# Optimization experiments

Hardware: AMD Instinct MI355X
Metric: run time of the kernel (lower is better)

Reference implementation:

```python
import jax, jax.numpy as jnp
import numpy as np

N_NODES = 100000


def _gcn_layer(x, src, dst, ew, norm_s, norm_d, W, b):
    # DGL GraphConv with edge weights, norm='both':
    # h_v = D_in(v)^-1/2 * sum_{(u,v) in E} w_uv * D_out(u)^-1/2 * x_u; then Linear.
    m = (x * norm_s[:, None])[src] * ew[:, None]        # [E, d] gather + weight
    agg = jax.ops.segment_sum(m, dst, num_segments=N_NODES)  # [N, d] scatter-add
    return (agg * norm_d[:, None]) @ W + b


def setup_inputs() -> dict:
    key = jax.random.key(0)
    ks = jax.random.split(key, 12)
    N, E, D, C = N_NODES, 1600000, 64, 32
    inp = {
        "x": jax.random.normal(ks[0], (N, D), jnp.float32),
        "src": jax.random.randint(ks[1], (E,), 0, N, jnp.int64),
        "dst": jax.random.randint(ks[2], (E,), 0, N, jnp.int64),
        "ew": jax.random.uniform(ks[3], (E,), jnp.float32),
    }
    s = 1.0 / np.sqrt(D)
    for i, k in zip(range(1, 5), ks[4:8]):
        inp[f"W{i}"] = jax.random.normal(k, (D, D), jnp.float32) * s
        inp[f"b{i}"] = jnp.zeros((D,), jnp.float32)
    inp["Wr"] = jax.random.normal(ks[8], (D, D), jnp.float32) * s
    inp["br"] = jnp.zeros((D,), jnp.float32)
    inp["Wo"] = jax.random.normal(ks[9], (D, C), jnp.float32) * s
    inp["bo"] = jnp.zeros((C,), jnp.float32)
    return inp


def reference(x, src, dst, ew, W1, b1, W2, b2, W3, b3, W4, b4, Wr, br, Wo, bo):
    ones = jnp.ones(src.shape, x.dtype)
    deg_out = jnp.clip(jax.ops.segment_sum(ones, src, num_segments=N_NODES), 1.0)
    deg_in = jnp.clip(jax.ops.segment_sum(ones, dst, num_segments=N_NODES), 1.0)
    norm_s = deg_out ** -0.5
    norm_d = deg_in ** -0.5

    res = x @ Wr + br
    h = jax.nn.relu(_gcn_layer(x, src, dst, ew, norm_s, norm_d, W1, b1))
    h = jax.nn.relu(_gcn_layer(h, src, dst, ew, norm_s, norm_d, W2, b2))
    h = jax.nn.relu(_gcn_layer(h, src, dst, ew, norm_s, norm_d, W3, b3))
    h = _gcn_layer(h, src, dst, ew, norm_s, norm_d, W4, b4)
    h = jax.nn.relu(h + res)
    return h @ Wo + bo
```

## Files before the change

### kernel.cpp

```cpp
#include <hip/hip_runtime.h>

#define NN 100000
#define D 64
#define G 3
#define RS 33334
#define NC 85
#define NB (G*NC)

typedef short bf16x8 __attribute__((ext_vector_type(8)));
typedef float f32x4 __attribute__((ext_vector_type(4)));
typedef float f32x2 __attribute__((ext_vector_type(2)));

__device__ __forceinline__ float bf2f_lo(unsigned w) { return __uint_as_float(w << 16); }
__device__ __forceinline__ float bf2f_hi(unsigned w) { return __uint_as_float(w & 0xffff0000u); }
__device__ __forceinline__ unsigned short f2bf(float f) {
    unsigned u = __float_as_uint(f);
    return (unsigned short)((u + 0x7fffu + ((u >> 16) & 1u)) >> 16);
}
__device__ __forceinline__ unsigned pack2(float a, float b) {
    return (unsigned)f2bf(a) | ((unsigned)f2bf(b) << 16);
}
__device__ __forceinline__ unsigned char f2fp8(float v) {
    return (unsigned char)(__builtin_amdgcn_cvt_pk_fp8_f32(v, v, 0, false) & 0xff);
}
__device__ __forceinline__ unsigned pack_cw(int s, float w) {
    return ((unsigned)f2bf(w) << 17) | (unsigned)s;
}
#define PKFMA(acc, w2, p) \
    asm("v_pk_fma_f32 %0, %1, %2, %0" : "+v"(acc) : "v"(w2), "v"(p))

__global__ __launch_bounds__(1024) void k_hist(const int* __restrict__ src,
                                               const int* __restrict__ dst,
                                               unsigned short* __restrict__ psd, int E) {
    __shared__ unsigned h[RS / 2];
    int b = blockIdx.x, t = threadIdx.x;
    int g = b / NC, c = b - g * NC;
    int lo = g * RS;
    for (int i = t; i < RS / 2; i += 1024) h[i] = 0;
    __syncthreads();
    int e0 = (int)((((long long)c * E / NC)) & ~3LL);
    int e1 = (c == NC - 1) ? E : (int)((((long long)(c + 1) * E / NC)) & ~3LL);
    int m = (e1 - e0) & ~4095;
    for (int e = e0 + t * 4; e < e0 + m; e += 4096) {
        int4 s4 = *(const int4*)(src + e);
        int4 d4 = *(const int4*)(dst + e);
        int v;
        v = s4.x - lo; if ((unsigned)v < RS) atomicAdd(&h[v >> 1], 1u << ((v & 1) * 16));
        v = s4.y - lo; if ((unsigned)v < RS) atomicAdd(&h[v >> 1], 1u << ((v & 1) * 16));
        v = s4.z - lo; if ((unsigned)v < RS) atomicAdd(&h[v >> 1], 1u << ((v & 1) * 16));
        v = s4.w - lo; if ((unsigned)v < RS) atomicAdd(&h[v >> 1], 1u << ((v & 1) * 16));
        v = d4.x - lo; if ((unsigned)v < RS) atomicAdd(&h[v >> 1], 1u << ((v & 1) * 16 + 8));
        v = d4.y - lo; if ((unsigned)v < RS) atomicAdd(&h[v >> 1], 1u << ((v & 1) * 16 + 8));
        v = d4.z - lo; if ((unsigned)v < RS) atomicAdd(&h[v >> 1], 1u << ((v & 1) * 16 + 8));
        v = d4.w - lo; if ((unsigned)v < RS) atomicAdd(&h[v >> 1], 1u << ((v & 1) * 16 + 8));
    }
    for (int e = e0 + m + t; e < e1; e += 1024) {
        int v = src[e] - lo; if ((unsigned)v < RS) atomicAdd(&h[v >> 1], 1u << ((v & 1) * 16));
        v = dst[e] - lo;     if ((unsigned)v < RS) atomicAdd(&h[v >> 1], 1u << ((v & 1) * 16 + 8));
    }
    __syncthreads();
    unsigned* pb = (unsigned*)(psd + (size_t)b * RS);
    for (int i = t; i < RS / 2; i += 1024) pb[i] = h[i];
}

__global__ __launch_bounds__(1024) void k_scan1m(const unsigned short* __restrict__ psd,
                                                 float* __restrict__ ns, float* __restrict__ nd,
                                                 int* __restrict__ rowptr,
                                                 int* __restrict__ bsum, int n) {
    __shared__ int lds[1024];
    int t = threadIdx.x;
    int i = blockIdx.x * 1024 + t;
    int sv = 0, dv = 0;
    if (i < n) {
        int g = i / RS, off = i - g * RS;
        const unsigned short* p = psd + (size_t)(g * NC) * RS + off;
        #pragma unroll 5
        for (int c = 0; c < NC; ++c) {
            unsigned v = p[(size_t)c * RS];
            sv += (int)(v & 0xffu);
            dv += (int)(v >> 8);
        }
        ns[i] = rsqrtf(fmaxf((float)sv, 1.0f));
        nd[i] = rsqrtf(fmaxf((float)dv, 1.0f));
    }
    lds[t] = dv;
    __syncthreads();
    for (int off = 1; off < 1024; off <<= 1) {
        int v = lds[t];
        int a = (t >= off) ? lds[t - off] : 0;
        __syncthreads();
        lds[t] = v + a;
        __syncthreads();
    }
    if (t == 1023) bsum[blockIdx.x] = lds[1023];
    if (i < n) rowptr[i] = lds[t] - dv;
}

__global__ void k_scan3c(int* __restrict__ rowptr, const int* __restrict__ bsum,
                         const unsigned short* __restrict__ psd,
                         unsigned short* __restrict__ cur16,
                         int n, int E, int nb) {
    __shared__ int sbs[128];
    int t = threadIdx.x;
    if (t < 128) sbs[t] = (t < nb) ? bsum[t] : 0;
    __syncthreads();
    for (int off = 1; off < 128; off <<= 1) {
        int v = 0, a = 0;
        if (t < 128) { v = sbs[t]; if (t >= off) a = sbs[t - off]; }
        __syncthreads();
        if (t < 128) sbs[t] = v + a;
        __syncthreads();
    }
    int i = blockIdx.x * blockDim.x + t;
    if (i == 0) rowptr[n] = E;
    if (i >= n) return;
    int blk = i >> 10;
    int base = (blk > 0) ? sbs[blk - 1] : 0;
    int r = rowptr[i] + base;
    rowptr[i] = r;
    int g = i / RS, off = i - g * RS;
    const unsigned short* p = psd + (size_t)(g * NC) * RS + off;
    unsigned short* cp = cur16 + (size_t)(g * NC) * RS + off;
    int run = 0;
    #pragma unroll 5
    for (int c = 0; c < NC; ++c) {
        cp[(size_t)c * RS] = (unsigned short)run;
        run += (int)(p[(size_t)c * RS] >> 8);
    }
}

__global__ __launch_bounds__(1024) void k_fillsort(const int* __restrict__ src,
                                                   const int* __restrict__ dst,
                                                   const float* __restrict__ ew,
                                                   const int* __restrict__ rowptr,
                                                   const unsigned short* __restrict__ cur16,
                                                   unsigned* __restrict__ cw, int E) {
    __shared__ int cur[RS];
    int b = blockIdx.x, t = threadIdx.x;
    int g = b / NC, c = b - g * NC;
    int lo = g * RS;
    const unsigned short* c16 = cur16 + (size_t)b * RS;
    for (int i = t; i < RS; i += 1024) cur[i] = rowptr[lo + i] + (int)c16[i];
    __syncthreads();
    int e0 = (int)((((long long)c * E / NC)) & ~3LL);
    int e1 = (c == NC - 1) ? E : (int)((((long long)(c + 1) * E / NC)) & ~3LL);
    int m = (e1 - e0) & ~4095;
    for (int e = e0 + t * 4; e < e0 + m; e += 4096) {
        int4 s4 = *(const int4*)(src + e);
        int4 d4 = *(const int4*)(dst + e);
        float4 w4 = *(const float4*)(ew + e);
        int d;
        d = d4.x - lo; if ((unsigned)d < RS) { int p = atomicAdd(&cur[d], 1); cw[p] = pack_cw(s4.x, w4.x); }
        d = d4.y - lo; if ((unsigned)d < RS) { int p = atomicAdd(&cur[d], 1); cw[p] = pack_cw(s4.y, w4.y); }
        d = d4.z - lo; if ((unsigned)d < RS) { int p = atomicAdd(&cur[d], 1); cw[p] = pack_cw(s4.z, w4.z); }
        d = d4.w - lo; if ((unsigned)d < RS) { int p = atomicAdd(&cur[d], 1); cw[p] = pack_cw(s4.w, w4.w); }
    }
    for (int e = e0 + m + t; e < e1; e += 1024) {
        int d = dst[e] - lo;
        if ((unsigned)d < RS) {
            int p = atomicAdd(&cur[d], 1);
            cw[p] = pack_cw(src[e], ew[e]);
        }
    }
}

__global__ __launch_bounds__(256) void k_gemm2(const float* __restrict__ x,
                                               const float* __restrict__ Wr,
                                               const float* __restrict__ brs,
                                               const float* __restrict__ W1,
                                               const float* __restrict__ ns,
                                               unsigned short* __restrict__ resb,
                                               unsigned char* __restrict__ tmat, int n) {
    __shared__ unsigned short WTr[64][72];
    __shared__ unsigned short WT1[64][72];
    int t = threadIdx.x;
    for (int i = t; i < 64 * 64; i += 256) {
        int k = i >> 6, nn = i & 63;
        WTr[nn][k] = f2bf(Wr[i]);
        WT1[nn][k] = f2bf(W1[i]);
    }
    __syncthreads();
    int w = t >> 6, lane = t & 63;
    int m = lane & 15, q = lane >> 4;
    int node0 = blockIdx.x * 64 + w * 16;
    int nodeA = min(node0 + m, n - 1);
    const float* inf = x + (size_t)nodeA * D;
    float sc = ns[nodeA];
    bf16x8 afr[2], afs[2];
    #pragma unroll
    for (int kc = 0; kc < 2; ++kc) {
        float4 f0 = *(const float4*)(inf + kc * 32 + q * 8);
        float4 f1 = *(const float4*)(inf + kc * 32 + q * 8 + 4);
        union { bf16x8 v; unsigned short u[8]; } ta, ts;
        ta.u[0] = f2bf(f0.x); ta.u[1] = f2bf(f0.y);
        ta.u[2] = f2bf(f0.z); ta.u[3] = f2bf(f0.w);
        ta.u[4] = f2bf(f1.x); ta.u[5] = f2bf(f1.y);
        ta.u[6] = f2bf(f1.z); ta.u[7] = f2bf(f1.w);
        ts.u[0] = f2bf(f0.x * sc); ts.u[1] = f2bf(f0.y * sc);
        ts.u[2] = f2bf(f0.z * sc); ts.u[3] = f2bf(f0.w * sc);
        ts.u[4] = f2bf(f1.x * sc); ts.u[5] = f2bf(f1.y * sc);
        ts.u[6] = f2bf(f1.z * sc); ts.u[7] = f2bf(f1.w * sc);
        afr[kc] = ta.v;
        afs[kc] = ts.v;
    }
    #pragma unroll
    for (int nt = 0; nt < 4; ++nt) {
        f32x4 ar = {0.f, 0.f, 0.f, 0.f};
        f32x4 at = {0.f, 0.f, 0.f, 0.f};
        #pragma unroll
        for (int kc = 0; kc < 2; ++kc) {
            union { bf16x8 v; uint4 u; } bfr, bf1;
            bfr.u = *(const uint4*)&WTr[nt * 16 + m][kc * 32 + q * 8];
            bf1.u = *(const uint4*)&WT1[nt * 16 + m][kc * 32 + q * 8];
            ar = __builtin_amdgcn_mfma_f32_16x16x32_bf16(afr[kc], bfr.v, ar, 0, 0, 0);
            at = __builtin_amdgcn_mfma_f32_16x16x32_bf16(afs[kc], bf1.v, at, 0, 0, 0);
        }
        int col = nt * 16 + m;
        float bb = brs[col];
        #pragma unroll
        for (int r = 0; r < 4; ++r) {
            int node = node0 + q * 4 + r;
            if (node < n) {
                resb[(size_t)node * D + col] = f2bf(ar[r] + bb);
                tmat[(size_t)node * D + col] = f2fp8(at[r]);
            }
        }
    }
}

template<bool LAST>
__global__ void k_gather(const int* __restrict__ rowptr, const unsigned* __restrict__ cw,
                         const unsigned char* __restrict__ tmat,
                         const float* __restrict__ nd, const float* __restrict__ ns,
                         const float* __restrict__ bias,
                         const unsigned short* __restrict__ resb,
                         unsigned short* __restrict__ outb, int n, int E) {
    int grp = threadIdx.x >> 3;
    int h   = threadIdx.x & 7;
    int node = blockIdx.x * 32 + grp;
    bool valid = node < n;
    int nc = valid ? node : 0;
    int beg = rowptr[nc];
    int end = valid ? rowptr[nc + 1] : beg;
    unsigned h8 = (unsigned)(h * 8);
    f32x2 A0={0.f,0.f},A1={0.f,0.f},A2={0.f,0.f},A3={0.f,0.f};
    f32x2 C0={0.f,0.f},C1={0.f,0.f},C2={0.f,0.f},C3={0.f,0.f};
    unsigned cv0 = (beg     < end) ? cw[beg]     : 0u;
    unsigned cv1 = (beg + 1 < end) ? cw[beg + 1] : 0u;
    unsigned cv2 = (beg + 2 < end) ? cw[beg + 2] : 0u;
    unsigned cv3 = (beg + 3 < end) ? cw[beg + 3] : 0u;
    unsigned cv4 = (beg + 4 < end) ? cw[beg + 4] : 0u;
    unsigned cv5 = (beg + 5 < end) ? cw[beg + 5] : 0u;
    unsigned cv6 = (beg + 6 < end) ? cw[beg + 6] : 0u;
    unsigned cv7 = (beg + 7 < end) ? cw[beg + 7] : 0u;
    for (int e = beg; e < end; e += 8) {
        uint2 r0 = *(const uint2*)(tmat + (((cv0 & 0x1FFFFu) << 6) + h8));
        uint2 r1 = *(const uint2*)(tmat + (((cv1 & 0x1FFFFu) << 6) + h8));
        uint2 r2 = *(const uint2*)(tmat + (((cv2 & 0x1FFFFu) << 6) + h8));
        uint2 r3 = *(const uint2*)(tmat + (((cv3 & 0x1FFFFu) << 6) + h8));
        uint2 r4 = *(const uint2*)(tmat + (((cv4 & 0x1FFFFu) << 6) + h8));
        uint2 r5 = *(const uint2*)(tmat + (((cv5 & 0x1FFFFu) << 6) + h8));
        uint2 r6 = *(const uint2*)(tmat + (((cv6 & 0x1FFFFu) << 6) + h8));
        uint2 r7 = *(const uint2*)(tmat + (((cv7 & 0x1FFFFu) << 6) + h8));
        float w0 = __uint_as_float((cv0 >> 17) << 16);
        float w1 = __uint_as_float((cv1 >> 17) << 16);
        float w2 = __uint_as_float((cv2 >> 17) << 16);
        float w3 = __uint_as_float((cv3 >> 17) << 16);
        float w4 = __uint_as_float((cv4 >> 17) << 16);
        float w5 = __uint_as_float((cv5 >> 17) << 16);
        float w6 = __uint_as_float((cv6 >> 17) << 16);
        float w7 = __uint_as_float((cv7 >> 17) << 16);
        int f = e + 8;
        cv0 = (f     < end) ? cw[f]     : 0u;
        cv1 = (f + 1 < end) ? cw[f + 1] : 0u;
        cv2 = (f + 2 < end) ? cw[f + 2] : 0u;
        cv3 = (f + 3 < end) ? cw[f + 3] : 0u;
        cv4 = (f + 4 < end) ? cw[f + 4] : 0u;
        cv5 = (f + 5 < end) ? cw[f + 5] : 0u;
        cv6 = (f + 6 < end) ? cw[f + 6] : 0u;
        cv7 = (f + 7 < end) ? cw[f + 7] : 0u;
        f32x2 p, wv;
        wv.x = w0; wv.y = w0;
        p = __builtin_amdgcn_cvt_pk_f32_fp8(r0.x, false); PKFMA(A0, wv, p);
        p = __builtin_amdgcn_cvt_pk_f32_fp8(r0.x, true);  PKFMA(A1, wv, p);
        p = __builtin_amdgcn_cvt_pk_f32_fp8(r0.y, false); PKFMA(A2, wv, p);
        p = __builtin_amdgcn_cvt_pk_f32_fp8(r0.y, true);  PKFMA(A3, wv, p);
        wv.x = w1; wv.y = w1;
        p = __builtin_amdgcn_cvt_pk_f32_fp8(r1.x, false); PKFMA(C0, wv, p);
        p = __builtin_amdgcn_cvt_pk_f32_fp8(r1.x, true);  PKFMA(C1, wv, p);
        p = __builtin_amdgcn_cvt_pk_f32_fp8(r1.y, false); PKFMA(C2, wv, p);
        p = __builtin_amdgcn_cvt_pk_f32_fp8(r1.y, true);  PKFMA(C3, wv, p);
        wv.x = w2; wv.y = w2;
        p = __builtin_amdgcn_cvt_pk_f32_fp8(r2.x, false); PKFMA(A0, wv, p);
        p = __builtin_amdgcn_cvt_pk_f32_fp8(r2.x, true);  PKFMA(A1, wv, p);
        p = __builtin_amdgcn_cvt_pk_f32_fp8(r2.y, false); PKFMA(A2, wv, p);
        p = __builtin_amdgcn_cvt_pk_f32_fp8(r2.y, true);  PKFMA(A3, wv, p);
        wv.x = w3; wv.y = w3;
        p = __builtin_amdgcn_cvt_pk_f32_fp8(r3.x, false); PKFMA(C0, wv, p);
        p = __builtin_amdgcn_cvt_pk_f32_fp8(r3.x, true);  PKFMA(C1, wv, p);
        p = __builtin_amdgcn_cvt_pk_f32_fp8(r3.y, false); PKFMA(C2, wv, p);
        p = __builtin_amdgcn_cvt_pk_f32_fp8(r3.y, true);  PKFMA(C3, wv, p);
        wv.x = w4; wv.y = w4;
        p = __builtin_amdgcn_cvt_pk_f32_fp8(r4.x, false); PKFMA(A0, wv, p);
        p = __builtin_amdgcn_cvt_pk_f32_fp8(r4.x, true);  PKFMA(A1, wv, p);
        p = __builtin_amdgcn_cvt_pk_f32_fp8(r4.y, false); PKFMA(A2, wv, p);
        p = __builtin_amdgcn_cvt_pk_f32_fp8(r4.y, true);  PKFMA(A3, wv, p);
        wv.x = w5; wv.y = w5;
        p = __builtin_amdgcn_cvt_pk_f32_fp8(r5.x, false); PKFMA(C0, wv, p);
        p = __builtin_amdgcn_cvt_pk_f32_fp8(r5.x, true);  PKFMA(C1, wv, p);
        p = __builtin_amdgcn_cvt_pk_f32_fp8(r5.y, false); PKFMA(C2, wv, p);
        p = __builtin_amdgcn_cvt_pk_f32_fp8(r5.y, true);  PKFMA(C3, wv, p);
        wv.x = w6; wv.y = w6;
        p = __builtin_amdgcn_cvt_pk_f32_fp8(r6.x, false); PKFMA(A0, wv, p);
        p = __builtin_amdgcn_cvt_pk_f32_fp8(r6.x, true);  PKFMA(A1, wv, p);
        p = __builtin_amdgcn_cvt_pk_f32_fp8(r6.y, false); PKFMA(A2, wv, p);
        p = __builtin_amdgcn_cvt_pk_f32_fp8(r6.y, true);  PKFMA(A3, wv, p);
        wv.x = w7; wv.y = w7;
        p = __builtin_amdgcn_cvt_pk_f32_fp8(r7.x, false); PKFMA(C0, wv, p);
        p = __builtin_amdgcn_cvt_pk_f32_fp8(r7.x, true);  PKFMA(C1, wv, p);
        p = __builtin_amdgcn_cvt_pk_f32_fp8(r7.y, false); PKFMA(C2, wv, p);
        p = __builtin_amdgcn_cvt_pk_f32_fp8(r7.y, true);  PKFMA(C3, wv, p);
    }
    if (!valid) return;
    float a0 = A0.x + C0.x, a1 = A0.y + C0.y;
    float a2 = A1.x + C1.x, a3 = A1.y + C1.y;
    float a4 = A2.x + C2.x, a5 = A2.y + C2.y;
    float a6 = A3.x + C3.x, a7 = A3.y + C3.y;
    float ndv = nd[node];
    float4 b0 = *(const float4*)(bias + 8 * h);
    float4 b1 = *(const float4*)(bias + 8 * h + 4);
    float v0 = ndv * a0 + b0.x, v1 = ndv * a1 + b0.y;
    float v2 = ndv * a2 + b0.z, v3 = ndv * a3 + b0.w;
    float v4 = ndv * a4 + b1.x, v5 = ndv * a5 + b1.y;
    float v6 = ndv * a6 + b1.z, v7 = ndv * a7 + b1.w;
    if (LAST) {
        uint4 r = *((const uint4*)(resb + (size_t)node * D) + h);
        v0 += bf2f_lo(r.x); v1 += bf2f_hi(r.x);
        v2 += bf2f_lo(r.y); v3 += bf2f_hi(r.y);
        v4 += bf2f_lo(r.z); v5 += bf2f_hi(r.z);
        v6 += bf2f_lo(r.w); v7 += bf2f_hi(r.w);
    }
    v0 = fmaxf(v0, 0.f); v1 = fmaxf(v1, 0.f); v2 = fmaxf(v2, 0.f); v3 = fmaxf(v3, 0.f);
    v4 = fmaxf(v4, 0.f); v5 = fmaxf(v5, 0.f); v6 = fmaxf(v6, 0.f); v7 = fmaxf(v7, 0.f);
    if (!LAST) {
        float s = ns[node];
        v0 *= s; v1 *= s; v2 *= s; v3 *= s; v4 *= s; v5 *= s; v6 *= s; v7 *= s;
    }
    uint4 o = make_uint4(pack2(v0, v1), pack2(v2, v3), pack2(v4, v5), pack2(v6, v7));
    *((uint4*)(outb + (size_t)node * D) + h) = o;
}

template<int OUTD, bool BIAS, int OUTMODE>
__global__ __launch_bounds__(256) void k_gemm(const unsigned short* __restrict__ inb,
                                              const float* __restrict__ W,
                                              const float* __restrict__ bias,
                                              void* __restrict__ out_, int n) {
    constexpr int NT = OUTD / 16;
    __shared__ unsigned short WT[OUTD][72];
    int t = threadIdx.x;
    for (int i = t; i < 64 * OUTD; i += 256) {
        int k = i / OUTD, nn = i % OUTD;
        WT[nn][k] = f2bf(W[i]);
    }
    __syncthreads();
    int w = t >> 6, lane = t & 63;
    int m = lane & 15, q = lane >> 4;
    int node0 = blockIdx.x * 64 + w * 16;
    int nodeA = min(node0 + m, n - 1);
    const unsigned short* ip = inb + (size_t)nodeA * D;
    bf16x8 afr[2];
    #pragma unroll
    for (int kc = 0; kc < 2; ++kc) {
        union { bf16x8 v; uint4 u; } tmp;
        tmp.u = *(const uint4*)(ip + kc * 32 + q * 8);
        afr[kc] = tmp.v;
    }
    #pragma unroll
    for (int nt = 0; nt < NT; ++nt) {
        f32x4 acc = {0.f, 0.f, 0.f, 0.f};
        #pragma unroll
        for (int kc = 0; kc < 2; ++kc) {
            union { bf16x8 v; uint4 u; } bfr;
            bfr.u = *(const uint4*)&WT[nt * 16 + m][kc * 32 + q * 8];
            acc = __builtin_amdgcn_mfma_f32_16x16x32_bf16(afr[kc], bfr.v, acc, 0, 0, 0);
        }
        int col = nt * 16 + m;
        float bb = BIAS ? bias[col] : 0.f;
        #pragma unroll
        for (int r = 0; r < 4; ++r) {
            int node = node0 + q * 4 + r;
            if (node < n) {
                float v = acc[r] + bb;
                if (OUTMODE == 2)
                    ((unsigned char*)out_)[(size_t)node * OUTD + col] = f2fp8(v);
                else
                    ((float*)out_)[(size_t)node * OUTD + col] = v;
            }
        }
    }
}

static inline char* align_up(char* p, size_t a) {
    return (char*)(((uintptr_t)p + a - 1) & ~(uintptr_t)(a - 1));
}

extern "C" void kernel_launch(void* const* d_in, const int* in_sizes, int n_in,
                              void* d_out, int out_size, void* d_ws, size_t ws_size,
                              hipStream_t stream) {
    const float* x   = (const float*)d_in[0];
    const int*   src = (const int*)d_in[1];
    const int*   dst = (const int*)d_in[2];
    const float* ew  = (const float*)d_in[3];
    const float* Wl[4] = {(const float*)d_in[4], (const float*)d_in[6],
                          (const float*)d_in[8], (const float*)d_in[10]};
    const float* bl[4] = {(const float*)d_in[5], (const float*)d_in[7],
                          (const float*)d_in[9], (const float*)d_in[11]};
    const float* Wr = (const float*)d_in[12];
    const float* br = (const float*)d_in[13];
    const float* Wo = (const float*)d_in[14];
    const float* bo = (const float*)d_in[15];
    float* out = (float*)d_out;

    const int N = NN;
    const int E = in_sizes[1];

    char* p = (char*)d_ws;
    float* norm_s = (float*)p;            p = align_up(p + N * 4, 256);
    float* norm_d = (float*)p;            p = align_up(p + N * 4, 256);
    int*   rowptr = (int*)p;              p = align_up(p + (size_t)(G * RS + 80) * 4, 256);
    int*   bsum   = (int*)p;              p = align_up(p + 128 * 4, 256);
    unsigned* cw  = (unsigned*)p;         p = align_up(p + (size_t)E * 4, 256);
    unsigned short* psd   = (unsigned short*)p; p = align_up(p + (size_t)NB * RS * 2, 256);
    unsigned short* cur16 = (unsigned short*)p; p = align_up(p + (size_t)NB * RS * 2, 256);
    unsigned short* resb  = (unsigned short*)p; p = align_up(p + (size_t)N * D * 2, 256);
    unsigned short* xs   = psd;
    unsigned char*  tmat = (unsigned char*)(xs + (size_t)N * D);

    k_hist<<<NB, 1024, 0, stream>>>(src, dst, psd, E);
    int nb = (N + 1023) / 1024;
    k_scan1m<<<nb, 1024, 0, stream>>>(psd, norm_s, norm_d, rowptr, bsum, N);
    k_scan3c<<<(N + 255) / 256, 256, 0, stream>>>(rowptr, bsum, psd, cur16, N, E, nb);
    k_fillsort<<<NB, 1024, 0, stream>>>(src, dst, ew, rowptr, cur16, cw, E);

    k_gemm2<<<(N + 63) / 64, 256, 0, stream>>>(x, Wr, br, Wl[0], norm_s, resb, tmat, N);

    k_gather<false><<<(N + 31) / 32, 256, 0, stream>>>(
        rowptr, cw, tmat, norm_d, norm_s, bl[0], nullptr, xs, N, E);
    k_gemm<64, false, 2><<<(N + 63) / 64, 256, 0, stream>>>(xs, Wl[1], nullptr, tmat, N);
    k_gather<false><<<(N + 31) / 32, 256, 0, stream>>>(
        rowptr, cw, tmat, norm_d, norm_s, bl[1], nullptr, xs, N, E);
    k_gemm<64, false, 2><<<(N + 63) / 64, 256, 0, stream>>>(xs, Wl[2], nullptr, tmat, N);
    k_gather<false><<<(N + 31) / 32, 256, 0, stream>>>(
        rowptr, cw, tmat, norm_d, norm_s, bl[2], nullptr, xs, N, E);
    k_gemm<64, false, 2><<<(N + 63) / 64, 256, 0, stream>>>(xs, Wl[3], nullptr, tmat, N);
    k_gather<true><<<(N + 31) / 32, 256, 0, stream>>>(
        rowptr, cw, tmat, norm_d, nullptr, bl[3], resb, xs, N, E);
    k_gemm<32, true, 0><<<(N + 63) / 64, 256, 0, stream>>>(xs, Wo, bo, out, N);
}
```

Before: 307.7 us.

## Pad CSR rows to multiples of eight to drop bounds checks in gather

```diff
diff --git a/kernel.cpp b/kernel.cpp
--- a/kernel.cpp
+++ b/kernel.cpp
@@ -83,7 +83,8 @@
         ns[i] = rsqrtf(fmaxf((float)sv, 1.0f));
         nd[i] = rsqrtf(fmaxf((float)dv, 1.0f));
     }
-    lds[t] = dv;
+    int dvp = (dv + 7) & ~7;
+    lds[t] = dvp;
     __syncthreads();
     for (int off = 1; off < 1024; off <<= 1) {
         int v = lds[t];
@@ -93,13 +94,14 @@
         __syncthreads();
     }
     if (t == 1023) bsum[blockIdx.x] = lds[1023];
-    if (i < n) rowptr[i] = lds[t] - dv;
+    if (i < n) rowptr[i] = lds[t] - dvp;
 }
 
 __global__ void k_scan3c(int* __restrict__ rowptr, const int* __restrict__ bsum,
                          const unsigned short* __restrict__ psd,
                          unsigned short* __restrict__ cur16,
-                         int n, int E, int nb) {
+                         unsigned* __restrict__ cw,
+                         int n, int nb) {
     __shared__ int sbs[128];
     int t = threadIdx.x;
     if (t < 128) sbs[t] = (t < nb) ? bsum[t] : 0;
@@ -112,7 +114,7 @@
         __syncthreads();
     }
     int i = blockIdx.x * blockDim.x + t;
-    if (i == 0) rowptr[n] = E;
+    if (i == 0) rowptr[n] = sbs[127];
     if (i >= n) return;
     int blk = i >> 10;
     int base = (blk > 0) ? sbs[blk - 1] : 0;
@@ -127,6 +129,8 @@
         cp[(size_t)c * RS] = (unsigned short)run;
         run += (int)(p[(size_t)c * RS] >> 8);
     }
+    int dp = (run + 7) & ~7;
+    for (int k = run; k < dp; ++k) cw[r + k] = 0u;
 }
 
 __global__ __launch_bounds__(1024) void k_fillsort(const int* __restrict__ src,
@@ -234,7 +238,7 @@
                          const float* __restrict__ nd, const float* __restrict__ ns,
                          const float* __restrict__ bias,
                          const unsigned short* __restrict__ resb,
-                         unsigned short* __restrict__ outb, int n, int E) {
+                         unsigned short* __restrict__ outb, int n) {
     int grp = threadIdx.x >> 3;
     int h   = threadIdx.x & 7;
     int node = blockIdx.x * 32 + grp;
@@ -245,14 +249,14 @@
     unsigned h8 = (unsigned)(h * 8);
     f32x2 A0={0.f,0.f},A1={0.f,0.f},A2={0.f,0.f},A3={0.f,0.f};
     f32x2 C0={0.f,0.f},C1={0.f,0.f},C2={0.f,0.f},C3={0.f,0.f};
-    unsigned cv0 = (beg     < end) ? cw[beg]     : 0u;
-    unsigned cv1 = (beg + 1 < end) ? cw[beg + 1] : 0u;
-    unsigned cv2 = (beg + 2 < end) ? cw[beg + 2] : 0u;
-    unsigned cv3 = (beg + 3 < end) ? cw[beg + 3] : 0u;
-    unsigned cv4 = (beg + 4 < end) ? cw[beg + 4] : 0u;
-    unsigned cv5 = (beg + 5 < end) ? cw[beg + 5] : 0u;
-    unsigned cv6 = (beg + 6 < end) ? cw[beg + 6] : 0u;
-    unsigned cv7 = (beg + 7 < end) ? cw[beg + 7] : 0u;
+    unsigned cv0 = cw[beg];
+    unsigned cv1 = cw[beg + 1];
+    unsigned cv2 = cw[beg + 2];
+    unsigned cv3 = cw[beg + 3];
+    unsigned cv4 = cw[beg + 4];
+    unsigned cv5 = cw[beg + 5];
+    unsigned cv6 = cw[beg + 6];
+    unsigned cv7 = cw[beg + 7];
     for (int e = beg; e < end; e += 8) {
         uint2 r0 = *(const uint2*)(tmat + (((cv0 & 0x1FFFFu) << 6) + h8));
         uint2 r1 = *(const uint2*)(tmat + (((cv1 & 0x1FFFFu) << 6) + h8));
@@ -271,14 +275,14 @@
         float w6 = __uint_as_float((cv6 >> 17) << 16);
         float w7 = __uint_as_float((cv7 >> 17) << 16);
         int f = e + 8;
-        cv0 = (f     < end) ? cw[f]     : 0u;
-        cv1 = (f + 1 < end) ? cw[f + 1] : 0u;
-        cv2 = (f + 2 < end) ? cw[f + 2] : 0u;
-        cv3 = (f + 3 < end) ? cw[f + 3] : 0u;
-        cv4 = (f + 4 < end) ? cw[f + 4] : 0u;
-        cv5 = (f + 5 < end) ? cw[f + 5] : 0u;
-        cv6 = (f + 6 < end) ? cw[f + 6] : 0u;
-        cv7 = (f + 7 < end) ? cw[f + 7] : 0u;
+        cv0 = cw[f];
+        cv1 = cw[f + 1];
+        cv2 = cw[f + 2];
+        cv3 = cw[f + 3];
+        cv4 = cw[f + 4];
+        cv5 = cw[f + 5];
+        cv6 = cw[f + 6];
+        cv7 = cw[f + 7];
         f32x2 p, wv;
         wv.x = w0; wv.y = w0;
         p = __builtin_amdgcn_cvt_pk_f32_fp8(r0.x, false); PKFMA(A0, wv, p);
@@ -429,7 +433,7 @@
     float* norm_d = (float*)p;            p = align_up(p + N * 4, 256);
     int*   rowptr = (int*)p;              p = align_up(p + (size_t)(G * RS + 80) * 4, 256);
     int*   bsum   = (int*)p;              p = align_up(p + 128 * 4, 256);
-    unsigned* cw  = (unsigned*)p;         p = align_up(p + (size_t)E * 4, 256);
+    unsigned* cw  = (unsigned*)p;         p = align_up(p + ((size_t)E + 7 * (size_t)N + 64) * 4, 256);
     unsigned short* psd   = (unsigned short*)p; p = align_up(p + (size_t)NB * RS * 2, 256);
     unsigned short* cur16 = (unsigned short*)p; p = align_up(p + (size_t)NB * RS * 2, 256);
     unsigned short* resb  = (unsigned short*)p; p = align_up(p + (size_t)N * D * 2, 256);
@@ -439,21 +443,21 @@
     k_hist<<<NB, 1024, 0, stream>>>(src, dst, psd, E);
     int nb = (N + 1023) / 1024;
     k_scan1m<<<nb, 1024, 0, stream>>>(psd, norm_s, norm_d, rowptr, bsum, N);
-    k_scan3c<<<(N + 255) / 256, 256, 0, stream>>>(rowptr, bsum, psd, cur16, N, E, nb);
+    k_scan3c<<<(N + 255) / 256, 256, 0, stream>>>(rowptr, bsum, psd, cur16, cw, N, nb);
     k_fillsort<<<NB, 1024, 0, stream>>>(src, dst, ew, rowptr, cur16, cw, E);
 
     k_gemm2<<<(N + 63) / 64, 256, 0, stream>>>(x, Wr, br, Wl[0], norm_s, resb, tmat, N);
 
     k_gather<false><<<(N + 31) / 32, 256, 0, stream>>>(
-        rowptr, cw, tmat, norm_d, norm_s, bl[0], nullptr, xs, N, E);
+        rowptr, cw, tmat, norm_d, norm_s, bl[0], nullptr, xs, N);
     k_gemm<64, false, 2><<<(N + 63) / 64, 256, 0, stream>>>(xs, Wl[1], nullptr, tmat, N);
     k_gather<false><<<(N + 31) / 32, 256, 0, stream>>>(
-        rowptr, cw, tmat, norm_d, norm_s, bl[1], nullptr, xs, N, E);
+        rowptr, cw, tmat, norm_d, norm_s, bl[1], nullptr, xs, N);
     k_gemm<64, false, 2><<<(N + 63) / 64, 256, 0, stream>>>(xs, Wl[2], nullptr, tmat, N);
     k_gather<false><<<(N + 31) / 32, 256, 0, stream>>>(
-        rowptr, cw, tmat, norm_d, norm_s, bl[2], nullptr, xs, N, E);
+        rowptr, cw, tmat, norm_d, norm_s, bl[2], nullptr, xs, N);
     k_gemm<64, false, 2><<<(N + 63) / 64, 256, 0, stream>>>(xs, Wl[3], nullptr, tmat, N);
     k_gather<true><<<(N + 31) / 32, 256, 0, stream>>>(
-        rowptr, cw, tmat, norm_d, nullptr, bl[3], resb, xs, N, E);
+        rowptr, cw, tmat, norm_d, nullptr, bl[3], resb, xs, N);
     k_gemm<32, true, 0><<<(N + 63) / 64, 256, 0, stream>>>(xs, Wo, bo, out, N);
 }
```

Measured after the change: 312.1 us. About the same (+1.4%).
